# Kernel optimization log

Measured on AMD Instinct MI355X. Metric: run time of the kernel, lower is better.

Reference implementation:

```python
import jax, jax.numpy as jnp
import numpy as np

NUM_EXPERTS = 8
DIM = 2048
BATCH = 8192


def setup_inputs() -> dict:
    key = jax.random.key(0)
    k_x, k_ids, k_w, k_b = jax.random.split(key, 4)
    x = jax.random.normal(k_x, (BATCH, DIM), dtype=jnp.float32)
    cam_pred_ids = jax.random.randint(k_ids, (BATCH,), 0, NUM_EXPERTS, dtype=jnp.int64)
    # torch nn.Linear default init: U(-1/sqrt(in), 1/sqrt(in)); W is [out, in]
    bound = 1.0 / np.sqrt(DIM)
    W = jax.random.uniform(k_w, (NUM_EXPERTS, DIM, DIM), dtype=jnp.float32,
                           minval=-bound, maxval=bound)
    b = jax.random.uniform(k_b, (NUM_EXPERTS, DIM), dtype=jnp.float32,
                           minval=-bound, maxval=bound)
    return {"x": x, "cam_pred_ids": cam_pred_ids, "W": W, "b": b}


def reference(x, cam_pred_ids, W, b):
    # Per-sample expert routing: out[i] = x[i] + relu(x[i] @ W[e].T + b[e]),
    # where e = cam_pred_ids[i]. Vectorized as 8 full-batch GEMMs with masked
    # combine (fixed small expert count -> Python loop is structural, not data).
    h = jnp.zeros_like(x)
    for e in range(NUM_EXPERTS):
        he = jax.nn.relu(x @ W[e].T + b[e])          # [B, D]
        mask = (cam_pred_ids == e)[:, None]
        h = h + jnp.where(mask, he, jnp.zeros((), dtype=x.dtype))
    return x + h
```

## Files before the change

kernel.cpp:

```cpp
#include <hip/hip_runtime.h>
#include <hip/hip_bf16.h>
#include <stdint.h>

#define BATCH 8192
#define DIM   2048
#define NEXP  8
#define BM    256
#define BN    128
#define BK    64
#define NKT   (DIM / BK)
#define MTILES 40
#define NBLK  (DIM / BN)
#define XHALF 4096
#define WCVTB 4096

typedef __bf16 bf16x8 __attribute__((ext_vector_type(8)));
typedef float  f32x4  __attribute__((ext_vector_type(4)));

#define XG_BYTE_OFF 40960ull
#define WB_BYTE_OFF 37789696ull
#define WS_NEED     104898560ull

#define AS1(p) ((const __attribute__((address_space(1))) void*)(p))
#define AS3(p) ((__attribute__((address_space(3))) void*)(p))

__device__ __forceinline__ unsigned f2bf2(float lo, float hi) {
    unsigned ul = __float_as_uint(lo), uh = __float_as_uint(hi);
    ul = (ul + 0x7FFFu + ((ul >> 16) & 1u)) >> 16;
    uh = (uh + 0x7FFFu + ((uh >> 16) & 1u)) >> 16;
    return (uh << 16) | ul;
}

__global__ __launch_bounds__(512)
void k_plan(const int* __restrict__ ids, int* __restrict__ ws,
            int* __restrict__ rowmap) {
    __shared__ int sc[512 * NEXP];
    __shared__ int seg[NEXP];
    __shared__ int tot[NEXP];
    int t = threadIdx.x;
    int myids[16];
    int base = t * 16;
#pragma unroll
    for (int e = 0; e < NEXP; e++) sc[t * NEXP + e] = 0;
#pragma unroll
    for (int i = 0; i < 16; i++) {
        myids[i] = ids[base + i];
        sc[t * NEXP + myids[i]]++;
    }
    __syncthreads();
    {
        int w = t >> 6, l = t & 63;
        int e = w;
        int vals[8], sum = 0;
#pragma unroll
        for (int j = 0; j < 8; j++) { vals[j] = sc[(l * 8 + j) * NEXP + e]; sum += vals[j]; }
        int inc = sum;
        for (int d = 1; d < 64; d <<= 1) {
            int v = __shfl_up(inc, d, 64);
            if (l >= d) inc += v;
        }
        int run = inc - sum;
#pragma unroll
        for (int j = 0; j < 8; j++) { int v = vals[j]; sc[(l * 8 + j) * NEXP + e] = run; run += v; }
        if (l == 63) tot[e] = run;
    }
    __syncthreads();
    if (t == 0) {
        int pos = 0, mt = 0;
        for (int e = 0; e < NEXP; e++) {
            int c = tot[e];
            seg[e] = pos;
            int ntl = (c + BM - 1) / BM;
            for (int tt = 0; tt < ntl; tt++) {
                ws[64  + mt] = e;
                ws[160 + mt] = pos + tt * BM;
                int v = c - tt * BM;
                ws[256 + mt] = v < BM ? v : BM;
                mt++;
            }
            pos += c;
        }
        ws[48] = mt;
    }
    __syncthreads();
#pragma unroll
    for (int i = 0; i < 16; i++) {
        int e = myids[i];
        int p = seg[e] + sc[t * NEXP + e]++;
        rowmap[p] = base + i;
    }
}

__global__ __launch_bounds__(256)
void k_prep(const float* __restrict__ x, const int* __restrict__ rowmap,
            unsigned short* __restrict__ xg,
            const float4* __restrict__ W, uint4* __restrict__ Wb) {
    int b = blockIdx.x;
    int t = threadIdx.x;
    if (b < XHALF) {
        int r0 = b * 2, r1 = r0 + 1;
        int m0 = rowmap[r0], m1 = rowmap[r1];
        const float4* s0 = (const float4*)(x + (size_t)m0 * DIM);
        const float4* s1 = (const float4*)(x + (size_t)m1 * DIM);
        float4 L0 = s0[2 * t], L1 = s0[2 * t + 1];
        float4 L2 = s1[2 * t], L3 = s1[2 * t + 1];
        uint4 v0, v1;
        v0.x = f2bf2(L0.x, L0.y); v0.y = f2bf2(L0.z, L0.w);
        v0.z = f2bf2(L1.x, L1.y); v0.w = f2bf2(L1.z, L1.w);
        v1.x = f2bf2(L2.x, L2.y); v1.y = f2bf2(L2.z, L2.w);
        v1.z = f2bf2(L3.x, L3.y); v1.w = f2bf2(L3.z, L3.w);
        ((uint4*)(xg + (size_t)r0 * DIM))[t] = v0;
        ((uint4*)(xg + (size_t)r1 * DIM))[t] = v1;
        return;
    }
    size_t base = (size_t)(b - XHALF) * 1024;
    float4 L[8];
#pragma unroll
    for (int k = 0; k < 4; k++) {
        size_t o = base + (size_t)k * 256 + t;
        L[2 * k]     = W[o * 2];
        L[2 * k + 1] = W[o * 2 + 1];
    }
#pragma unroll
    for (int k = 0; k < 4; k++) {
        size_t o = base + (size_t)k * 256 + t;
        uint4 v;
        v.x = f2bf2(L[2 * k].x,     L[2 * k].y);
        v.y = f2bf2(L[2 * k].z,     L[2 * k].w);
        v.z = f2bf2(L[2 * k + 1].x, L[2 * k + 1].y);
        v.w = f2bf2(L[2 * k + 1].z, L[2 * k + 1].w);
        Wb[o] = v;
    }
}

__global__ __launch_bounds__(512)
void k_gemm(const unsigned short* __restrict__ xg,
            const unsigned short* __restrict__ Wb,
            const float* __restrict__ bias,
            const int* __restrict__ ws, const int* __restrict__ rowmap,
            float* __restrict__ out) {
    int mt = blockIdx.y;
    if (mt >= ws[48]) return;
    int e     = ws[64  + mt];
    int pos0  = ws[160 + mt];
    int valid = ws[256 + mt];
    int n0 = blockIdx.x * BN;

    __shared__ __align__(16) unsigned char lds[3 * 49152];

    int tid = threadIdx.x;
    int w = tid >> 6, l = tid & 63;
    int l15 = l & 15, quad = l >> 4, x7 = l15 & 7;
    int wm = (w >> 1) * 64, wn = (w & 1) * 64;

    const unsigned short* Abase = xg + (size_t)pos0 * DIM;
    const unsigned short* Bbase = Wb + ((size_t)e * DIM + n0) * DIM;

    int srcA[4], srcB[2];
#pragma unroll
    for (int j = 0; j < 4; j++) {
        int g = w * 256 + j * 64 + l;
        int row = g >> 3, pos = g & 7;
        srcA[j] = row * DIM + (pos ^ (row & 7)) * 8;
    }
#pragma unroll
    for (int j = 0; j < 2; j++) {
        int h = w * 128 + j * 64 + l;
        int row = h >> 3, pos = h & 7;
        srcB[j] = row * DIM + (pos ^ (row & 7)) * 8;
    }
    int dA0 = (w * 256) * 16;
    int dB0 = 32768 + (w * 128) * 16;

    int aOff[2][4], bOff[2][4];
#pragma unroll
    for (int s = 0; s < 2; s++) {
        int ph = ((s * 4 + quad) ^ x7) * 16;
#pragma unroll
        for (int i = 0; i < 4; i++) {
            aOff[s][i] = (wm + i * 16 + l15) * 128 + ph;
            bOff[s][i] = 32768 + (wn + i * 16 + l15) * 128 + ph;
        }
    }

    f32x4 acc[4][4];
#pragma unroll
    for (int i = 0; i < 4; i++)
#pragma unroll
        for (int j = 0; j < 4; j++) acc[i][j] = (f32x4){0.f, 0.f, 0.f, 0.f};

#define GL(srcp, dstoff)                                                        \
    __builtin_amdgcn_global_load_lds(AS1(srcp), AS3(lds + (dstoff)), 16, 0, 0)
#define STAGE_P0(bb, k0)                                                        \
    do {                                                                        \
        GL(Abase + (k0) + srcA[0], (bb) + dA0);                                 \
        GL(Abase + (k0) + srcA[1], (bb) + dA0 + 1024);                          \
        GL(Bbase + (k0) + srcB[0], (bb) + dB0);                                 \
    } while (0)
#define STAGE_P1(bb, k0)                                                        \
    do {                                                                        \
        GL(Abase + (k0) + srcA[2], (bb) + dA0 + 2048);                          \
        GL(Abase + (k0) + srcA[3], (bb) + dA0 + 3072);                          \
        GL(Bbase + (k0) + srcB[1], (bb) + dB0 + 1024);                          \
    } while (0)

    STAGE_P0(0, 0);        STAGE_P1(0, 0);
    STAGE_P0(49152, BK);   STAGE_P1(49152, BK);
    asm volatile("s_waitcnt vmcnt(6)" ::: "memory");
    __builtin_amdgcn_s_barrier();

    int cur = 0;
    for (int kt = 0; kt < NKT; ++kt) {
        const unsigned char* pb = lds + cur * 49152;
        int pre = cur + 2; if (pre >= 3) pre -= 3;
        int preb = pre * 49152;
        int k2 = (kt + 2) * BK;
        bool dopre = (kt + 2 < NKT);
        {
            bf16x8 af[4], bf[4];
#pragma unroll
            for (int i = 0; i < 4; i++) af[i] = *(const bf16x8*)(pb + aOff[0][i]);
#pragma unroll
            for (int i = 0; i < 4; i++) bf[i] = *(const bf16x8*)(pb + bOff[0][i]);
            if (dopre) STAGE_P0(preb, k2);
            __builtin_amdgcn_s_barrier();
            asm volatile("s_waitcnt lgkmcnt(0)" ::: "memory");
            __builtin_amdgcn_sched_barrier(0);
            __builtin_amdgcn_s_setprio(1);
#pragma unroll
            for (int mi = 0; mi < 4; mi++)
#pragma unroll
                for (int ni = 0; ni < 4; ni++)
                    acc[mi][ni] = __builtin_amdgcn_mfma_f32_16x16x32_bf16(
                        af[mi], bf[ni], acc[mi][ni], 0, 0, 0);
            __builtin_amdgcn_s_setprio(0);
            __builtin_amdgcn_s_barrier();
        }
        {
            bf16x8 af[4], bf[4];
#pragma unroll
            for (int i = 0; i < 4; i++) af[i] = *(const bf16x8*)(pb + aOff[1][i]);
#pragma unroll
            for (int i = 0; i < 4; i++) bf[i] = *(const bf16x8*)(pb + bOff[1][i]);
            if (dopre) STAGE_P1(preb, k2);
            if (kt < NKT - 2) asm volatile("s_waitcnt vmcnt(6)" ::: "memory");
            else              asm volatile("s_waitcnt vmcnt(0)" ::: "memory");
            __builtin_amdgcn_sched_barrier(0);
            __builtin_amdgcn_s_barrier();
            asm volatile("s_waitcnt lgkmcnt(0)" ::: "memory");
            __builtin_amdgcn_sched_barrier(0);
            __builtin_amdgcn_s_setprio(1);
#pragma unroll
            for (int mi = 0; mi < 4; mi++)
#pragma unroll
                for (int ni = 0; ni < 4; ni++)
                    acc[mi][ni] = __builtin_amdgcn_mfma_f32_16x16x32_bf16(
                        af[mi], bf[ni], acc[mi][ni], 0, 0, 0);
            __builtin_amdgcn_s_setprio(0);
            __builtin_amdgcn_s_barrier();
        }
        cur += 1; if (cur == 3) cur = 0;
    }
#undef GL
#undef STAGE_P0
#undef STAGE_P1

    float bv[4];
#pragma unroll
    for (int ni = 0; ni < 4; ni++)
        bv[ni] = bias[(size_t)e * DIM + n0 + wn + ni * 16 + l15];
#pragma unroll
    for (int mi = 0; mi < 4; mi++) {
#pragma unroll
        for (int r4 = 0; r4 < 4; r4++) {
            int rl = wm + mi * 16 + quad * 4 + r4;
            if (rl < valid) {
                int orig = rowmap[pos0 + rl];
                const unsigned short* xrow = xg + (size_t)(pos0 + rl) * DIM + n0;
                float* orow = out + (size_t)orig * DIM + n0;
#pragma unroll
                for (int ni = 0; ni < 4; ni++) {
                    int col = wn + ni * 16 + l15;
                    float xv = __uint_as_float((unsigned)xrow[col] << 16);
                    float v = acc[mi][ni][r4] + bv[ni];
                    v = v > 0.f ? v : 0.f;
                    orow[col] = xv + v;
                }
            }
        }
    }
}

__global__ void k_naive(const float* __restrict__ x, const int* __restrict__ ids,
                        const float* __restrict__ W, const float* __restrict__ b,
                        float* __restrict__ out) {
    __shared__ float lx[DIM];
    int i = blockIdx.x;
    for (int t = threadIdx.x; t < DIM; t += blockDim.x) lx[t] = x[(size_t)i * DIM + t];
    __syncthreads();
    int e = ids[i];
    const float* We = W + (size_t)e * DIM * DIM;
    for (int n = threadIdx.x; n < DIM; n += blockDim.x) {
        const float* wr = We + (size_t)n * DIM;
        float acc = 0.f;
        for (int k = 0; k < DIM; k += 4) {
            float4 w4 = *(const float4*)(wr + k);
            acc += lx[k] * w4.x + lx[k + 1] * w4.y + lx[k + 2] * w4.z + lx[k + 3] * w4.w;
        }
        float v = acc + b[(size_t)e * DIM + n];
        v = v > 0.f ? v : 0.f;
        out[(size_t)i * DIM + n] = lx[n] + v;
    }
}

extern "C" void kernel_launch(void* const* d_in, const int* in_sizes, int n_in,
                              void* d_out, int out_size, void* d_ws, size_t ws_size,
                              hipStream_t stream) {
    const float* x   = (const float*)d_in[0];
    const int*   ids = (const int*)d_in[1];
    const float* W   = (const float*)d_in[2];
    const float* b   = (const float*)d_in[3];
    float* out = (float*)d_out;

    if (ws_size < WS_NEED) {
        k_naive<<<BATCH, 256, 0, stream>>>(x, ids, W, b, out);
        return;
    }

    char* wsb = (char*)d_ws;
    int*  wsi = (int*)wsb;
    int* rowmap = wsi + 512;
    unsigned short* xg = (unsigned short*)(wsb + XG_BYTE_OFF);
    unsigned short* Wb = (unsigned short*)(wsb + WB_BYTE_OFF);

    k_plan<<<1, 512, 0, stream>>>(ids, wsi, rowmap);
    k_prep<<<XHALF + WCVTB, 256, 0, stream>>>(x, rowmap, xg,
                                              (const float4*)W, (uint4*)Wb);
    dim3 g(NBLK, MTILES);
    k_gemm<<<g, 512, 0, stream>>>(xg, Wb, b, wsi, rowmap, out);
}
```

Before: 389.7 us.

## Switch GEMM to BK=32 with six-stage LDS ring and one barrier per step

```diff
diff --git a/kernel.cpp b/kernel.cpp
--- a/kernel.cpp
+++ b/kernel.cpp
@@ -7,8 +7,8 @@
 #define NEXP  8
 #define BM    256
 #define BN    128
-#define BK    64
-#define NKT   (DIM / BK)
+#define BK    32
+#define NITER (DIM / BK)
 #define MTILES 40
 #define NBLK  (DIM / BN)
 #define XHALF 4096
@@ -146,41 +146,37 @@
     int valid = ws[256 + mt];
     int n0 = blockIdx.x * BN;
 
-    __shared__ __align__(16) unsigned char lds[3 * 49152];
+    __shared__ __align__(16) unsigned char lds[6 * 24576];
 
     int tid = threadIdx.x;
     int w = tid >> 6, l = tid & 63;
-    int l15 = l & 15, quad = l >> 4, x7 = l15 & 7;
+    int l15 = l & 15, quad = l >> 4;
     int wm = (w >> 1) * 64, wn = (w & 1) * 64;
 
     const unsigned short* Abase = xg + (size_t)pos0 * DIM;
     const unsigned short* Bbase = Wb + ((size_t)e * DIM + n0) * DIM;
 
-    int srcA[4], srcB[2];
-#pragma unroll
-    for (int j = 0; j < 4; j++) {
-        int g = w * 256 + j * 64 + l;
-        int row = g >> 3, pos = g & 7;
-        srcA[j] = row * DIM + (pos ^ (row & 7)) * 8;
-    }
+    int srcA[2], srcB0;
 #pragma unroll
     for (int j = 0; j < 2; j++) {
-        int h = w * 128 + j * 64 + l;
-        int row = h >> 3, pos = h & 7;
-        srcB[j] = row * DIM + (pos ^ (row & 7)) * 8;
-    }
-    int dA0 = (w * 256) * 16;
-    int dB0 = 32768 + (w * 128) * 16;
-
-    int aOff[2][4], bOff[2][4];
-#pragma unroll
-    for (int s = 0; s < 2; s++) {
-        int ph = ((s * 4 + quad) ^ x7) * 16;
-#pragma unroll
-        for (int i = 0; i < 4; i++) {
-            aOff[s][i] = (wm + i * 16 + l15) * 128 + ph;
-            bOff[s][i] = 32768 + (wn + i * 16 + l15) * 128 + ph;
-        }
+        int g = w * 128 + j * 64 + l;
+        int row = g >> 2, pos = g & 3;
+        srcA[j] = row * DIM + (pos ^ ((row >> 1) & 3)) * 8;
+    }
+    {
+        int h = w * 64 + l;
+        int row = h >> 2, pos = h & 3;
+        srcB0 = row * DIM + (pos ^ ((row >> 1) & 3)) * 8;
+    }
+    int dA0 = w * 2048;
+    int dB0 = 16384 + w * 1024;
+
+    int swz = (quad ^ ((l15 >> 1) & 3)) * 16;
+    int aOff[4], bOff[4];
+#pragma unroll
+    for (int i = 0; i < 4; i++) {
+        aOff[i] = (wm + i * 16 + l15) * 64 + swz;
+        bOff[i] = 16384 + (wn + i * 16 + l15) * 64 + swz;
     }
 
     f32x4 acc[4][4];
@@ -191,79 +187,58 @@
 
 #define GL(srcp, dstoff)                                                        \
     __builtin_amdgcn_global_load_lds(AS1(srcp), AS3(lds + (dstoff)), 16, 0, 0)
-#define STAGE_P0(bb, k0)                                                        \
+#define STAGE(bb, k0)                                                           \
     do {                                                                        \
         GL(Abase + (k0) + srcA[0], (bb) + dA0);                                 \
         GL(Abase + (k0) + srcA[1], (bb) + dA0 + 1024);                          \
-        GL(Bbase + (k0) + srcB[0], (bb) + dB0);                                 \
+        GL(Bbase + (k0) + srcB0,  (bb) + dB0);                                  \
     } while (0)
-#define STAGE_P1(bb, k0)                                                        \
+#define VMCNT(NSTR) asm volatile("s_waitcnt vmcnt(" NSTR ")" ::: "memory")
+
+#define BODY(ktv, curb, DOPRE, preb, NSTR)                                      \
     do {                                                                        \
-        GL(Abase + (k0) + srcA[2], (bb) + dA0 + 2048);                          \
-        GL(Abase + (k0) + srcA[3], (bb) + dA0 + 3072);                          \
-        GL(Bbase + (k0) + srcB[1], (bb) + dB0 + 1024);                          \
+        VMCNT(NSTR);                                                            \
+        __builtin_amdgcn_s_barrier();                                           \
+        __builtin_amdgcn_sched_barrier(0);                                      \
+        const unsigned char* pb = lds + (curb);                                 \
+        bf16x8 af[4], bf[4];                                                    \
+        _Pragma("unroll")                                                       \
+        for (int i_ = 0; i_ < 4; i_++) af[i_] = *(const bf16x8*)(pb + aOff[i_]);\
+        _Pragma("unroll")                                                       \
+        for (int i_ = 0; i_ < 4; i_++) bf[i_] = *(const bf16x8*)(pb + bOff[i_]);\
+        if (DOPRE) STAGE(preb, ((ktv) + 5) * BK);                               \
+        asm volatile("s_waitcnt lgkmcnt(0)" ::: "memory");                      \
+        __builtin_amdgcn_sched_barrier(0);                                      \
+        __builtin_amdgcn_s_setprio(1);                                          \
+        _Pragma("unroll")                                                       \
+        for (int mi_ = 0; mi_ < 4; mi_++)                                       \
+            _Pragma("unroll")                                                   \
+            for (int ni_ = 0; ni_ < 4; ni_++)                                   \
+                acc[mi_][ni_] = __builtin_amdgcn_mfma_f32_16x16x32_bf16(        \
+                    af[mi_], bf[ni_], acc[mi_][ni_], 0, 0, 0);                  \
+        __builtin_amdgcn_s_setprio(0);                                          \
     } while (0)
 
-    STAGE_P0(0, 0);        STAGE_P1(0, 0);
-    STAGE_P0(49152, BK);   STAGE_P1(49152, BK);
-    asm volatile("s_waitcnt vmcnt(6)" ::: "memory");
-    __builtin_amdgcn_s_barrier();
-
-    int cur = 0;
-    for (int kt = 0; kt < NKT; ++kt) {
-        const unsigned char* pb = lds + cur * 49152;
-        int pre = cur + 2; if (pre >= 3) pre -= 3;
-        int preb = pre * 49152;
-        int k2 = (kt + 2) * BK;
-        bool dopre = (kt + 2 < NKT);
-        {
-            bf16x8 af[4], bf[4];
-#pragma unroll
-            for (int i = 0; i < 4; i++) af[i] = *(const bf16x8*)(pb + aOff[0][i]);
-#pragma unroll
-            for (int i = 0; i < 4; i++) bf[i] = *(const bf16x8*)(pb + bOff[0][i]);
-            if (dopre) STAGE_P0(preb, k2);
-            __builtin_amdgcn_s_barrier();
-            asm volatile("s_waitcnt lgkmcnt(0)" ::: "memory");
-            __builtin_amdgcn_sched_barrier(0);
-            __builtin_amdgcn_s_setprio(1);
-#pragma unroll
-            for (int mi = 0; mi < 4; mi++)
-#pragma unroll
-                for (int ni = 0; ni < 4; ni++)
-                    acc[mi][ni] = __builtin_amdgcn_mfma_f32_16x16x32_bf16(
-                        af[mi], bf[ni], acc[mi][ni], 0, 0, 0);
-            __builtin_amdgcn_s_setprio(0);
-            __builtin_amdgcn_s_barrier();
-        }
-        {
-            bf16x8 af[4], bf[4];
-#pragma unroll
-            for (int i = 0; i < 4; i++) af[i] = *(const bf16x8*)(pb + aOff[1][i]);
-#pragma unroll
-            for (int i = 0; i < 4; i++) bf[i] = *(const bf16x8*)(pb + bOff[1][i]);
-            if (dopre) STAGE_P1(preb, k2);
-            if (kt < NKT - 2) asm volatile("s_waitcnt vmcnt(6)" ::: "memory");
-            else              asm volatile("s_waitcnt vmcnt(0)" ::: "memory");
-            __builtin_amdgcn_sched_barrier(0);
-            __builtin_amdgcn_s_barrier();
-            asm volatile("s_waitcnt lgkmcnt(0)" ::: "memory");
-            __builtin_amdgcn_sched_barrier(0);
-            __builtin_amdgcn_s_setprio(1);
-#pragma unroll
-            for (int mi = 0; mi < 4; mi++)
-#pragma unroll
-                for (int ni = 0; ni < 4; ni++)
-                    acc[mi][ni] = __builtin_amdgcn_mfma_f32_16x16x32_bf16(
-                        af[mi], bf[ni], acc[mi][ni], 0, 0, 0);
-            __builtin_amdgcn_s_setprio(0);
-            __builtin_amdgcn_s_barrier();
-        }
-        cur += 1; if (cur == 3) cur = 0;
-    }
+#pragma unroll
+    for (int t5 = 0; t5 < 5; ++t5) STAGE(t5 * 24576, t5 * BK);
+
+    {
+        int cur = 0;
+        for (int kt = 0; kt < NITER - 5; ++kt) {
+            int pre = (cur == 0) ? 5 : cur - 1;
+            BODY(kt, cur * 24576, true, pre * 24576, "12");
+            cur = (cur == 5) ? 0 : cur + 1;
+        }
+    }
+    BODY(NITER - 5, ((NITER - 5) % 6) * 24576, false, 0, "12");
+    BODY(NITER - 4, ((NITER - 4) % 6) * 24576, false, 0, "9");
+    BODY(NITER - 3, ((NITER - 3) % 6) * 24576, false, 0, "6");
+    BODY(NITER - 2, ((NITER - 2) % 6) * 24576, false, 0, "3");
+    BODY(NITER - 1, ((NITER - 1) % 6) * 24576, false, 0, "0");
+#undef BODY
+#undef VMCNT
+#undef STAGE
 #undef GL
-#undef STAGE_P0
-#undef STAGE_P1
 
     float bv[4];
 #pragma unroll
```

Result: slower. 399.8 us (+2.6%).
